# Kernel optimization log

Hardware: AMD Instinct MI355X
Metric: run time of the kernel (lower is better)

Reference implementation:

```python
import jax, jax.numpy as jnp
import numpy as np

B, T, S, SYM, FFT = 256, 4, 2, 14, 128   # batch, num_tx, streams_per_tx, ofdm symbols, fft size
NSC, GUARD = 108, 10                      # effective subcarriers, guard offset
L = SYM * NSC                             # 1512, de-mash matrix dimension


def setup_inputs() -> dict:
    key = jax.random.key(0)
    k1, k2, k3, k4 = jax.random.split(key, 4)
    scale = 1.0 / np.sqrt(L).astype(np.float32)  # keep C roughly unitary-scaled
    return {
        "x_real": jax.random.normal(k1, (B, T, S, SYM, FFT), jnp.float32),
        "x_imag": jax.random.normal(k2, (B, T, S, SYM, FFT), jnp.float32),
        "C_real": jax.random.normal(k3, (L, L), jnp.float32) * scale,
        "C_imag": jax.random.normal(k4, (L, L), jnp.float32) * scale,
        "sc_ind": jnp.arange(NSC, dtype=jnp.int32) + GUARD,  # effective subcarrier indices
    }


def reference(x_real, x_imag, C_real, C_imag, sc_ind):
    # Complex RG and de-mash matrix
    x = jax.lax.complex(x_real, x_imag)           # [B,T,S,SYM,FFT] complex64
    C = jax.lax.complex(C_real, C_imag)           # [L,L] complex64

    # gather effective subcarriers along last axis
    y = jnp.take(x, sc_ind, axis=-1)              # [B,T,S,SYM,NSC]
    b, t, s, sym, nsc = y.shape

    # flatten_last_dims(y, 2) and multiply from right by C^H (adjoint=True)
    yf = y.reshape(b, t, s, sym * nsc)            # [B,T,S,L]
    yf = jnp.einsum('btsl,ml->btsm', yf, jnp.conj(C))  # y @ C^H
    y = yf.reshape(b, t, s, sym, nsc)             # [B,T,S,SYM,NSC]

    # scatter back into the full grid (equivalent to the transpose/scatter_nd/transpose chain,
    # since sc_ind is unique and the scatter is along the subcarrier axis)
    out = jnp.zeros(x.shape, x.dtype).at[..., sc_ind].set(y)

    # return real/imag stacked so the output is a single float32 array
    return jnp.stack([out.real, out.imag], axis=0)  # [2,B,T,S,SYM,FFT]
```

## Files before the change

kernel.cpp:

```cpp
#include <hip/hip_runtime.h>
#include <cstdint>
#include <cstddef>


typedef _Float16 half_t;
typedef half_t half8 __attribute__((ext_vector_type(8)));
typedef half_t half4 __attribute__((ext_vector_type(4)));
typedef half_t half2_t __attribute__((ext_vector_type(2)));
typedef float floatx4 __attribute__((ext_vector_type(4)));
typedef float floatv4 __attribute__((ext_vector_type(4)));

#define M_DIM 2048
#define K_DIM 3072
#define L_PAD 1536
#define N2_DIM 1536
#define LDIM 1512
#define NSC 108
#define SYMS 14
#define FFT 128
#define ROWLEN (SYMS * FFT)

#define BM 64
#define BN 64
#define BK 32
#define NITER (L_PAD / BK)

#define PA2_BLOCKS 6048
#define PW2_BLOCKS 4608
#define PAP_BLOCKS 48
#define PG_BLOCKS 4480
#define PREP_BLOCKS (PA2_BLOCKS + PW2_BLOCKS + PAP_BLOCKS + PG_BLOCKS)

typedef __attribute__((address_space(3))) uint32_t lds_u32_t;
typedef const __attribute__((address_space(1))) uint32_t glob_u32_t;

__device__ __forceinline__ void gl2lds16(const void* g, void* l) {
    __builtin_amdgcn_global_load_lds((glob_u32_t*)g, (lds_u32_t*)l, 16, 0, 0);
}

__global__ __launch_bounds__(256) void prep_all(
    const float* __restrict__ xr, const float* __restrict__ xi,
    const float* __restrict__ Cr, const float* __restrict__ Ci,
    const int* __restrict__ sc,
    half_t* __restrict__ A, half_t* __restrict__ W, float* __restrict__ out)
{
    const int b = blockIdx.x;
    const int t = threadIdx.x;

    if (b < PA2_BLOCKS) {
        int idx = b * 256 + t;
        int jp = idx % 54;
        int rest = idx / 54;
        int sym = rest % 14;
        int row = rest / 14;
        int s0 = sc[2 * jp];
        int s1 = sc[2 * jp + 1];
        const float* xrp = xr + (size_t)row * ROWLEN + sym * FFT;
        const float* xip = xi + (size_t)row * ROWLEN + sym * FFT;
        half2_t hr = { (half_t)xrp[s0], (half_t)xrp[s1] };
        half2_t hi = { (half_t)xip[s0], (half_t)xip[s1] };
        size_t dst = (size_t)row * K_DIM + sym * NSC + 2 * jp;
        *(half2_t*)(A + dst) = hr;
        *(half2_t*)(A + dst + L_PAD) = hi;
    } else if (b < PA2_BLOCKS + PW2_BLOCKS) {
        int idx = (b - PA2_BLOCKS) * 256 + t;
        int kq = idx % 768;
        int n = idx / 768;
        int k0 = kq * 4;
        floatv4 f = {0.0f, 0.0f, 0.0f, 0.0f};
        if (n < LDIM) {
            if (k0 < L_PAD) {
                if (k0 < LDIM)
                    f = *(const floatv4*)(Cr + (size_t)n * LDIM + k0);
            } else {
                int l = k0 - L_PAD;
                if (l < LDIM)
                    f = *(const floatv4*)(Ci + (size_t)n * LDIM + l);
            }
        }
        half4 h = { (half_t)f.x, (half_t)f.y, (half_t)f.z, (half_t)f.w };
        *(half4*)(W + (size_t)n * K_DIM + k0) = h;
    } else if (b < PA2_BLOCKS + PW2_BLOCKS + PAP_BLOCKS) {
        int idx = (b - PA2_BLOCKS - PW2_BLOCKS) * 256 + t;
        int c = idx % 6;
        int row = idx / 6;
        int col = (c < 3) ? (LDIM + c * 8) : (L_PAD + LDIM + (c - 3) * 8);
        half8 z = {};
        *(half8*)(A + (size_t)row * K_DIM + col) = z;
    } else {
        int idx = (b - PA2_BLOCKS - PW2_BLOCKS - PAP_BLOCKS) * 256 + t;
        int c20 = idx % 20;
        int rest = idx / 20;
        int sym = rest % 14;
        int rowri = rest / 14;
        int col = (c20 < 10) ? c20 : (NSC + c20);
        out[(size_t)rowri * ROWLEN + sym * FFT + col] = 0.0f;
    }
}

__global__ __launch_bounds__(256, 3) void gemm_scatter(
    const half_t* __restrict__ A,
    const half_t* __restrict__ W,
    const int* __restrict__ sc,
    float* __restrict__ out)
{
    __shared__ __align__(16) half_t As[2][BM * 2 * BK];
    __shared__ __align__(16) half_t Ws[2][BN * 2 * BK];

    const int t = threadIdx.x;
    const int bn = blockIdx.x;
    const int bm = blockIdx.y;
    const int lane = t & 63;
    const int w = t >> 6;
    const int wm = (w >> 1) * 32;
    const int wn = (w & 1) * 32;

    floatx4 aRR[2][2] = {}, aII[2][2] = {}, aIR[2][2] = {}, aRI[2][2] = {};

    const half_t* gA[2];
    const half_t* gW[2];
    int lOff[2];
#pragma unroll
    for (int r = 0; r < 2; ++r) {
        int c = r * 256 + t;
        int row = c >> 3, slot = c & 7;
        int g = slot ^ (row & 7);
        int gcol = (g < 4) ? g * 8 : (L_PAD + (g - 4) * 8);
        gA[r] = A + (size_t)(bm * BM + row) * K_DIM + gcol;
        gW[r] = W + (size_t)(bn * BN + row) * K_DIM + gcol;
        lOff[r] = c * 8;
    }

    const int fr = lane & 15;
    const int cr = lane >> 4;
    const int sR = (cr ^ (fr & 7)) * 8;
    const int sI = ((4 + cr) ^ (fr & 7)) * 8;

#pragma unroll
    for (int r = 0; r < 2; ++r) {
        gl2lds16(gA[r], &As[0][lOff[r]]);
        gl2lds16(gW[r], &Ws[0][lOff[r]]);
        gA[r] += BK; gW[r] += BK;
    }
    __syncthreads();

    for (int kb = 0; kb < NITER; ++kb) {
        const int nb = kb & 1;
        if (kb < NITER - 1) {
#pragma unroll
            for (int r = 0; r < 2; ++r) {
                gl2lds16(gA[r], &As[nb ^ 1][lOff[r]]);
                gl2lds16(gW[r], &Ws[nb ^ 1][lOff[r]]);
                gA[r] += BK; gW[r] += BK;
            }
        }

        half8 yr[2], yi[2], cRf[2], cIf[2];
#pragma unroll
        for (int i = 0; i < 2; ++i) {
            const half_t* rb = &As[nb][(wm + i * 16 + fr) * (2 * BK)];
            yr[i] = *(const half8*)(rb + sR);
            yi[i] = *(const half8*)(rb + sI);
        }
#pragma unroll
        for (int j = 0; j < 2; ++j) {
            const half_t* rb = &Ws[nb][(wn + j * 16 + fr) * (2 * BK)];
            cRf[j] = *(const half8*)(rb + sR);
            cIf[j] = *(const half8*)(rb + sI);
        }
#pragma unroll
        for (int i = 0; i < 2; ++i)
#pragma unroll
            for (int j = 0; j < 2; ++j) {
                aRR[i][j] = __builtin_amdgcn_mfma_f32_16x16x32_f16(
                    yr[i], cRf[j], aRR[i][j], 0, 0, 0);
                aII[i][j] = __builtin_amdgcn_mfma_f32_16x16x32_f16(
                    yi[i], cIf[j], aII[i][j], 0, 0, 0);
                aIR[i][j] = __builtin_amdgcn_mfma_f32_16x16x32_f16(
                    yi[i], cRf[j], aIR[i][j], 0, 0, 0);
                aRI[i][j] = __builtin_amdgcn_mfma_f32_16x16x32_f16(
                    yr[i], cIf[j], aRI[i][j], 0, 0, 0);
            }
        __syncthreads();
    }

    const int rq = lane >> 4;
#pragma unroll
    for (int j = 0; j < 2; ++j) {
        int n = bn * BN + wn + j * 16 + fr;
        if (n >= LDIM) continue;
        int sym = n / NSC;
        int jj = n - sym * NSC;
        size_t colR = (size_t)sym * FFT + sc[jj];
        size_t colI = (size_t)M_DIM * ROWLEN + colR;
#pragma unroll
        for (int i = 0; i < 2; ++i) {
            int m0 = bm * BM + wm + i * 16 + rq * 4;
#pragma unroll
            for (int r = 0; r < 4; ++r) {
                float vr = aRR[i][j][r] + aII[i][j][r];
                float vi = aIR[i][j][r] - aRI[i][j][r];
                out[colR + (size_t)(m0 + r) * ROWLEN] = vr;
                out[colI + (size_t)(m0 + r) * ROWLEN] = vi;
            }
        }
    }
}

extern "C" void kernel_launch(void* const* d_in, const int* in_sizes, int n_in,
                              void* d_out, int out_size, void* d_ws, size_t ws_size,
                              hipStream_t stream) {
    const float* xr = (const float*)d_in[0];
    const float* xi = (const float*)d_in[1];
    const float* Cr = (const float*)d_in[2];
    const float* Ci = (const float*)d_in[3];
    const int* sc   = (const int*)d_in[4];
    float* out = (float*)d_out;

    half_t* Ah = (half_t*)d_ws;
    half_t* Wh = (half_t*)((char*)d_ws + (size_t)M_DIM * K_DIM * 2);

    prep_all<<<PREP_BLOCKS, 256, 0, stream>>>(
        xr, xi, Cr, Ci, sc, Ah, Wh, out);

    dim3 grid(N2_DIM / BN, M_DIM / BM);
    gemm_scatter<<<grid, 256, 0, stream>>>(Ah, Wh, sc, out);
}
```

Measured before the change: 153.0 us.

## Use single-buffered BK=96 K-tiles with XCD-aware block remapping in GEMM

The K tile grows from 32 to 96, so there are fewer loop iterations and barriers. Double buffering is dropped in favour of a single LDS buffer filled synchronously each iteration. The grid becomes a 1D launch of 768 blocks, remapped so that consecutive blocks on the same XCD share tiles, which is meant to improve L2 locality. Without double buffering, global loads no longer overlap compute, so latency may be exposed unless enough blocks stay resident per CU to hide it.

```diff
diff --git a/kernel.cpp b/kernel.cpp
--- a/kernel.cpp
+++ b/kernel.cpp
@@ -22,8 +22,10 @@
 
 #define BM 64
 #define BN 64
-#define BK 32
+#define BK 96
 #define NITER (L_PAD / BK)
+#define ROWH (2 * BK)
+#define CPR 24
 
 #define PA2_BLOCKS 6048
 #define PW2_BLOCKS 4608
@@ -104,12 +106,14 @@
     const int* __restrict__ sc,
     float* __restrict__ out)
 {
-    __shared__ __align__(16) half_t As[2][BM * 2 * BK];
-    __shared__ __align__(16) half_t Ws[2][BN * 2 * BK];
+    __shared__ __align__(16) half_t As[BM * ROWH];
+    __shared__ __align__(16) half_t Ws[BN * ROWH];
 
     const int t = threadIdx.x;
-    const int bn = blockIdx.x;
-    const int bm = blockIdx.y;
+    const int bid = blockIdx.x;
+    const int nbid = (bid & 7) * 96 + (bid >> 3);
+    const int bn = nbid % 24;
+    const int bm = nbid / 24;
     const int lane = t & 63;
     const int w = t >> 6;
     const int wm = (w >> 1) * 32;
@@ -117,15 +121,15 @@
 
     floatx4 aRR[2][2] = {}, aII[2][2] = {}, aIR[2][2] = {}, aRI[2][2] = {};
 
-    const half_t* gA[2];
-    const half_t* gW[2];
-    int lOff[2];
-#pragma unroll
-    for (int r = 0; r < 2; ++r) {
+    const half_t* gA[6];
+    const half_t* gW[6];
+    int lOff[6];
+#pragma unroll
+    for (int r = 0; r < 6; ++r) {
         int c = r * 256 + t;
-        int row = c >> 3, slot = c & 7;
-        int g = slot ^ (row & 7);
-        int gcol = (g < 4) ? g * 8 : (L_PAD + (g - 4) * 8);
+        int row = c / CPR, slot = c % CPR;
+        int g = (slot & ~7) | ((slot & 7) ^ (row & 7));
+        int gcol = (g < 12) ? g * 8 : (L_PAD + (g - 12) * 8);
         gA[r] = A + (size_t)(bm * BM + row) * K_DIM + gcol;
         gW[r] = W + (size_t)(bn * BN + row) * K_DIM + gcol;
         lOff[r] = c * 8;
@@ -133,55 +137,52 @@
 
     const int fr = lane & 15;
     const int cr = lane >> 4;
-    const int sR = (cr ^ (fr & 7)) * 8;
-    const int sI = ((4 + cr) ^ (fr & 7)) * 8;
-
-#pragma unroll
-    for (int r = 0; r < 2; ++r) {
-        gl2lds16(gA[r], &As[0][lOff[r]]);
-        gl2lds16(gW[r], &Ws[0][lOff[r]]);
-        gA[r] += BK; gW[r] += BK;
-    }
-    __syncthreads();
+    const int frl = fr & 7;
 
     for (int kb = 0; kb < NITER; ++kb) {
-        const int nb = kb & 1;
-        if (kb < NITER - 1) {
-#pragma unroll
-            for (int r = 0; r < 2; ++r) {
-                gl2lds16(gA[r], &As[nb ^ 1][lOff[r]]);
-                gl2lds16(gW[r], &Ws[nb ^ 1][lOff[r]]);
-                gA[r] += BK; gW[r] += BK;
-            }
-        }
-
-        half8 yr[2], yi[2], cRf[2], cIf[2];
-#pragma unroll
-        for (int i = 0; i < 2; ++i) {
-            const half_t* rb = &As[nb][(wm + i * 16 + fr) * (2 * BK)];
-            yr[i] = *(const half8*)(rb + sR);
-            yi[i] = *(const half8*)(rb + sI);
-        }
-#pragma unroll
-        for (int j = 0; j < 2; ++j) {
-            const half_t* rb = &Ws[nb][(wn + j * 16 + fr) * (2 * BK)];
-            cRf[j] = *(const half8*)(rb + sR);
-            cIf[j] = *(const half8*)(rb + sI);
-        }
-#pragma unroll
-        for (int i = 0; i < 2; ++i)
+        __syncthreads();
+#pragma unroll
+        for (int r = 0; r < 6; ++r) {
+            gl2lds16(gA[r], &As[lOff[r]]);
+            gl2lds16(gW[r], &Ws[lOff[r]]);
+        }
+#pragma unroll
+        for (int r = 0; r < 6; ++r) { gA[r] += BK; gW[r] += BK; }
+        __syncthreads();
+
+#pragma unroll
+        for (int ss = 0; ss < 3; ++ss) {
+            const int qR = ss * 4 + cr;
+            const int qI = 12 + ss * 4 + cr;
+            const int sR = ((qR & ~7) | ((qR & 7) ^ frl)) * 8;
+            const int sI = ((qI & ~7) | ((qI & 7) ^ frl)) * 8;
+            half8 yr[2], yi[2], cRf[2], cIf[2];
+#pragma unroll
+            for (int i = 0; i < 2; ++i) {
+                const half_t* rb = &As[(wm + i * 16 + fr) * ROWH];
+                yr[i] = *(const half8*)(rb + sR);
+                yi[i] = *(const half8*)(rb + sI);
+            }
 #pragma unroll
             for (int j = 0; j < 2; ++j) {
-                aRR[i][j] = __builtin_amdgcn_mfma_f32_16x16x32_f16(
-                    yr[i], cRf[j], aRR[i][j], 0, 0, 0);
-                aII[i][j] = __builtin_amdgcn_mfma_f32_16x16x32_f16(
-                    yi[i], cIf[j], aII[i][j], 0, 0, 0);
-                aIR[i][j] = __builtin_amdgcn_mfma_f32_16x16x32_f16(
-                    yi[i], cRf[j], aIR[i][j], 0, 0, 0);
-                aRI[i][j] = __builtin_amdgcn_mfma_f32_16x16x32_f16(
-                    yr[i], cIf[j], aRI[i][j], 0, 0, 0);
-            }
-        __syncthreads();
+                const half_t* rb = &Ws[(wn + j * 16 + fr) * ROWH];
+                cRf[j] = *(const half8*)(rb + sR);
+                cIf[j] = *(const half8*)(rb + sI);
+            }
+#pragma unroll
+            for (int i = 0; i < 2; ++i)
+#pragma unroll
+                for (int j = 0; j < 2; ++j) {
+                    aRR[i][j] = __builtin_amdgcn_mfma_f32_16x16x32_f16(
+                        yr[i], cRf[j], aRR[i][j], 0, 0, 0);
+                    aII[i][j] = __builtin_amdgcn_mfma_f32_16x16x32_f16(
+                        yi[i], cIf[j], aII[i][j], 0, 0, 0);
+                    aIR[i][j] = __builtin_amdgcn_mfma_f32_16x16x32_f16(
+                        yi[i], cRf[j], aIR[i][j], 0, 0, 0);
+                    aRI[i][j] = __builtin_amdgcn_mfma_f32_16x16x32_f16(
+                        yr[i], cIf[j], aRI[i][j], 0, 0, 0);
+                }
+        }
     }
 
     const int rq = lane >> 4;
@@ -223,6 +224,5 @@
     prep_all<<<PREP_BLOCKS, 256, 0, stream>>>(
         xr, xi, Cr, Ci, sc, Ah, Wh, out);
 
-    dim3 grid(N2_DIM / BN, M_DIM / BM);
-    gemm_scatter<<<grid, 256, 0, stream>>>(Ah, Wh, sc, out);
-}
+    gemm_scatter<<<768, 256, 0, stream>>>(Ah, Wh, sc, out);
+}
```

Measured after the change: 147.0 us. 1.04x faster.
